# Kernel tuning notes

Hardware: AMD Instinct MI355X
Metric: run time of the kernel (lower is better)

## Reference

```python
import jax, jax.numpy as jnp
import numpy as np

IN_DIMS = 512
TOKEN_DIM = 512
NUM_HEADS = 1
D = TOKEN_DIM * NUM_HEADS
SCALE = TOKEN_DIM ** (-0.5)
EPS = 1e-12  # torch F.normalize default


def _l2norm(v, axis):
    n = jnp.sqrt(jnp.sum(v * v, axis=axis, keepdims=True))
    return v / jnp.maximum(n, EPS)


def setup_inputs() -> dict:
    key = jax.random.key(0)
    ks = jax.random.split(key, 10)
    B, C, H, W = 64, IN_DIMS, 28, 28
    s_in = IN_DIMS ** -0.5
    s_d = D ** -0.5
    return {
        "x": jax.random.normal(ks[0], (B, C, H, W), jnp.float32),
        "Wq": jax.random.normal(ks[1], (IN_DIMS, D), jnp.float32) * s_in,
        "bq": jax.random.normal(ks[2], (D,), jnp.float32) * 0.01,
        "Wk": jax.random.normal(ks[3], (IN_DIMS, D), jnp.float32) * s_in,
        "bk": jax.random.normal(ks[4], (D,), jnp.float32) * 0.01,
        "w_g": jax.random.normal(ks[5], (D, 1), jnp.float32),
        "Wp": jax.random.normal(ks[6], (D, D), jnp.float32) * s_d,
        "bp": jax.random.normal(ks[7], (D,), jnp.float32) * 0.01,
        "Wf": jax.random.normal(ks[8], (D, TOKEN_DIM), jnp.float32) * s_d,
        "bf": jax.random.normal(ks[9], (TOKEN_DIM,), jnp.float32) * 0.01,
    }


def reference(x, Wq, bq, Wk, bk, w_g, Wp, bp, Wf, bf):
    B, C, H, W = x.shape
    t = x.reshape(B, C, H * W).transpose(0, 2, 1)          # [B, N, C]
    query = _l2norm(t @ Wq + bq, axis=-1)                  # [B, N, D]
    k = _l2norm(t @ Wk + bk, axis=-1)                      # [B, N, D]
    attn = _l2norm((query @ w_g) * SCALE, axis=1)          # [B, N, 1], normalized over tokens
    ctx = jnp.sum(attn * query, axis=1, keepdims=True)     # [B, 1, D] global context
    out = (ctx * k) @ Wp + bp + query                      # [B, N, D]
    out = out @ Wf + bf                                    # [B, N, TOKEN_DIM]
    return out.transpose(0, 2, 1).reshape(B, -1, H, W)
```

## Files before the change

### kernel.cpp

```cpp
#include <hip/hip_runtime.h>

#define EPSN 1e-12f
#define SCALE_F 0.044194173824159216f

typedef __bf16 bf16x8 __attribute__((ext_vector_type(8)));
typedef float  f32x4  __attribute__((ext_vector_type(4)));

__global__ __launch_bounds__(256) void k_prep_t(const float* __restrict__ Wq,
                                                const float* __restrict__ Wk,
                                                __bf16* __restrict__ WqT,
                                                __bf16* __restrict__ WkT) {
  int idx = blockIdx.x * 256 + threadIdx.x;
  int d = idx >> 9, c = idx & 511;
  WqT[idx] = (__bf16)Wq[c * 512 + d];
  WkT[idx] = (__bf16)Wk[c * 512 + d];
}

__global__ __launch_bounds__(512) void k_prep_w(const float* __restrict__ Wp,
                                                const float* __restrict__ Wf,
                                                const float* __restrict__ bp,
                                                const float* __restrict__ bfv,
                                                __bf16* __restrict__ WcT,
                                                float* __restrict__ bpf) {
  int kk = blockIdx.x;
  int d  = threadIdx.x;
  float acc = 0.f;
  for (int c = 0; c < 512; ++c) acc = fmaf(Wp[kk * 512 + c], Wf[c * 512 + d], acc);
  WcT[(size_t)d * 1024 + kk]       = (__bf16)acc;
  WcT[(size_t)d * 1024 + 512 + kk] = (__bf16)Wf[kk * 512 + d];
  if (kk == 0) {
    float a2 = 0.f;
    for (int c = 0; c < 512; ++c) a2 = fmaf(bp[c], Wf[c * 512 + d], a2);
    bpf[d] = a2 + bfv[d];
  }
}

__global__ __launch_bounds__(512) void k_qk(const float* __restrict__ x,
                                            const __bf16* __restrict__ WqT,
                                            const __bf16* __restrict__ WkT,
                                            const float* __restrict__ bq,
                                            const float* __restrict__ bk,
                                            const float* __restrict__ wg,
                                            __bf16* __restrict__ Qn,
                                            __bf16* __restrict__ Kn,
                                            float* __restrict__ g) {
  __shared__ __bf16 As[64][40];
  __shared__ float redQ[8][64], redK[8][64], redG[8][64];
  __shared__ float invq[64], invk[64];
  const int t = threadIdx.x;
  const int lane = t & 63, w = t >> 6;
  const int li = lane & 15, lq = lane >> 4;
  const int n0 = blockIdx.x * 64;
  const int b  = blockIdx.y;
  const int sn = t & 63;
  const int sc = t >> 6;
  f32x4 accQ[4][4] = {}, accK[4][4] = {};
  for (int ks = 0; ks < 16; ++ks) {
    const int c0 = ks * 32;
    #pragma unroll
    for (int p = 0; p < 4; ++p) {
      int c = sc + p * 8;
      float v = 0.f;
      if (n0 + sn < 784) v = x[((size_t)b * 512 + c0 + c) * 784 + n0 + sn];
      As[sn][c] = (__bf16)v;
    }
    __syncthreads();
    bf16x8 af[4];
    #pragma unroll
    for (int rb = 0; rb < 4; ++rb)
      af[rb] = *(const bf16x8*)&As[rb * 16 + li][lq * 8];
    #pragma unroll
    for (int cb = 0; cb < 4; ++cb) {
      const int drow = w * 64 + cb * 16 + li;
      bf16x8 bqf = *(const bf16x8*)(WqT + (size_t)drow * 512 + c0 + lq * 8);
      bf16x8 bkf = *(const bf16x8*)(WkT + (size_t)drow * 512 + c0 + lq * 8);
      #pragma unroll
      for (int rb = 0; rb < 4; ++rb) {
        accQ[rb][cb] = __builtin_amdgcn_mfma_f32_16x16x32_bf16(af[rb], bqf, accQ[rb][cb], 0, 0, 0);
        accK[rb][cb] = __builtin_amdgcn_mfma_f32_16x16x32_bf16(af[rb], bkf, accK[rb][cb], 0, 0, 0);
      }
    }
    __syncthreads();
  }
  float bqv[4], bkv[4], wgv[4];
  #pragma unroll
  for (int cb = 0; cb < 4; ++cb) {
    int col = w * 64 + cb * 16 + li;
    bqv[cb] = bq[col]; bkv[cb] = bk[col]; wgv[cb] = wg[col];
  }
  #pragma unroll
  for (int rb = 0; rb < 4; ++rb)
    #pragma unroll
    for (int cb = 0; cb < 4; ++cb)
      #pragma unroll
      for (int j = 0; j < 4; ++j) {
        accQ[rb][cb][j] += bqv[cb];
        accK[rb][cb][j] += bkv[cb];
      }
  #pragma unroll
  for (int rb = 0; rb < 4; ++rb)
    #pragma unroll
    for (int j = 0; j < 4; ++j) {
      float sq = 0.f, sk = 0.f, sg = 0.f;
      #pragma unroll
      for (int cb = 0; cb < 4; ++cb) {
        float vq = accQ[rb][cb][j], vk = accK[rb][cb][j];
        sq = fmaf(vq, vq, sq); sk = fmaf(vk, vk, sk); sg = fmaf(vq, wgv[cb], sg);
      }
      sq += __shfl_xor(sq, 1); sq += __shfl_xor(sq, 2); sq += __shfl_xor(sq, 4); sq += __shfl_xor(sq, 8);
      sk += __shfl_xor(sk, 1); sk += __shfl_xor(sk, 2); sk += __shfl_xor(sk, 4); sk += __shfl_xor(sk, 8);
      sg += __shfl_xor(sg, 1); sg += __shfl_xor(sg, 2); sg += __shfl_xor(sg, 4); sg += __shfl_xor(sg, 8);
      if (li == 0) {
        int row = rb * 16 + lq * 4 + j;
        redQ[w][row] = sq; redK[w][row] = sk; redG[w][row] = sg;
      }
    }
  __syncthreads();
  if (t < 64) {
    float sq = 0.f, sk = 0.f, sg = 0.f;
    #pragma unroll
    for (int wv = 0; wv < 8; ++wv) { sq += redQ[wv][t]; sk += redK[wv][t]; sg += redG[wv][t]; }
    float iq = 1.f / fmaxf(sqrtf(sq), EPSN);
    float ik = 1.f / fmaxf(sqrtf(sk), EPSN);
    invq[t] = iq; invk[t] = ik;
    if (n0 + t < 784) g[(size_t)b * 784 + n0 + t] = sg * iq;
  }
  __syncthreads();
  #pragma unroll
  for (int rb = 0; rb < 4; ++rb)
    #pragma unroll
    for (int j = 0; j < 4; ++j) {
      int row = rb * 16 + lq * 4 + j;
      if (n0 + row < 784) {
        float iq = invq[row], ik = invk[row];
        size_t base = ((size_t)b * 784 + n0 + row) * 512 + w * 64 + li;
        #pragma unroll
        for (int cb = 0; cb < 4; ++cb) {
          Qn[base + cb * 16] = (__bf16)(accQ[rb][cb][j] * iq);
          Kn[base + cb * 16] = (__bf16)(accK[rb][cb][j] * ik);
        }
      }
    }
}

__global__ __launch_bounds__(512) void k_ctx(const __bf16* __restrict__ Qn,
                                             const float* __restrict__ g,
                                             float* __restrict__ ctx) {
  const int b = blockIdx.x, t = threadIdx.x;
  __shared__ float wred[8];
  const float* gb = g + (size_t)b * 784;
  float s = 0.f;
  for (int n = t; n < 784; n += 512) { float v = gb[n]; s = fmaf(v, v, s); }
  s += __shfl_xor(s, 1);  s += __shfl_xor(s, 2);  s += __shfl_xor(s, 4);
  s += __shfl_xor(s, 8);  s += __shfl_xor(s, 16); s += __shfl_xor(s, 32);
  if ((t & 63) == 0) wred[t >> 6] = s;
  __syncthreads();
  float tot = 0.f;
  #pragma unroll
  for (int i = 0; i < 8; ++i) tot += wred[i];
  float alpha = SCALE_F / fmaxf(sqrtf(tot) * SCALE_F, EPSN);
  const __bf16* qb = Qn + (size_t)b * 784 * 512;
  float a0 = 0.f, a1 = 0.f, a2 = 0.f, a3 = 0.f;
  for (int n = 0; n < 784; n += 4) {
    a0 = fmaf(gb[n],     (float)qb[(size_t)n * 512 + t],       a0);
    a1 = fmaf(gb[n + 1], (float)qb[(size_t)(n + 1) * 512 + t], a1);
    a2 = fmaf(gb[n + 2], (float)qb[(size_t)(n + 2) * 512 + t], a2);
    a3 = fmaf(gb[n + 3], (float)qb[(size_t)(n + 3) * 512 + t], a3);
  }
  ctx[(size_t)b * 512 + t] = alpha * ((a0 + a1) + (a2 + a3));
}

__global__ __launch_bounds__(512) void k_out(const __bf16* __restrict__ Qn,
                                             const __bf16* __restrict__ Kn,
                                             const float* __restrict__ ctx,
                                             const __bf16* __restrict__ WcT,
                                             const float* __restrict__ bpf,
                                             float* __restrict__ out) {
  __shared__ __align__(16) char smem[64 * 72 * 2 + 256 * 72 * 2];
  __bf16 (*As)[72] = (__bf16(*)[72])smem;
  __bf16 (*Bs)[72] = (__bf16(*)[72])(smem + 64 * 72 * 2);
  float  (*Cs)[65] = (float(*)[65])smem;
  const int t = threadIdx.x;
  const int lane = t & 63, w = t >> 6;
  const int li = lane & 15, lq = lane >> 4;
  const int wr = w >> 2, wc = w & 3;
  const int n0 = blockIdx.x * 64;
  const int d0 = blockIdx.y * 256;
  const int b  = blockIdx.z;
  const int arow = t >> 3, asg = t & 7;
  f32x4 acc[2][4] = {};
  for (int ks = 0; ks < 16; ++ks) {
    const int k0 = ks * 64;
    {
      int kk = k0 + asg * 8;
      int n = n0 + arow;
      bf16x8 v = {};
      if (kk < 512) {
        if (n < 784) v = *(const bf16x8*)(Kn + ((size_t)b * 784 + n) * 512 + kk);
        const float* cp = ctx + b * 512 + kk;
        bf16x8 r;
        #pragma unroll
        for (int j = 0; j < 8; ++j) r[j] = (__bf16)((float)v[j] * cp[j]);
        *(bf16x8*)&As[arow][asg * 8] = r;
      } else {
        if (n < 784) v = *(const bf16x8*)(Qn + ((size_t)b * 784 + n) * 512 + kk - 512);
        *(bf16x8*)&As[arow][asg * 8] = v;
      }
    }
    #pragma unroll
    for (int p = 0; p < 4; ++p) {
      int d = (t >> 3) + p * 64;
      *(bf16x8*)&Bs[d][asg * 8] = *(const bf16x8*)(WcT + (size_t)(d0 + d) * 1024 + k0 + asg * 8);
    }
    __syncthreads();
    bf16x8 af[2][2], bfr[4][2];
    #pragma unroll
    for (int rb = 0; rb < 2; ++rb)
      #pragma unroll
      for (int kf = 0; kf < 2; ++kf)
        af[rb][kf] = *(const bf16x8*)&As[wr * 32 + rb * 16 + li][kf * 32 + lq * 8];
    #pragma unroll
    for (int cb = 0; cb < 4; ++cb)
      #pragma unroll
      for (int kf = 0; kf < 2; ++kf)
        bfr[cb][kf] = *(const bf16x8*)&Bs[wc * 64 + cb * 16 + li][kf * 32 + lq * 8];
    #pragma unroll
    for (int kf = 0; kf < 2; ++kf)
      #pragma unroll
      for (int rb = 0; rb < 2; ++rb)
        #pragma unroll
        for (int cb = 0; cb < 4; ++cb)
          acc[rb][cb] = __builtin_amdgcn_mfma_f32_16x16x32_bf16(af[rb][kf], bfr[cb][kf], acc[rb][cb], 0, 0, 0);
    __syncthreads();
  }
  for (int ch = 0; ch < 4; ++ch) {
    if (wc == ch) {
      #pragma unroll
      for (int cb = 0; cb < 4; ++cb) {
        int colL = cb * 16 + li;
        float bias = bpf[d0 + ch * 64 + colL];
        #pragma unroll
        for (int rb = 0; rb < 2; ++rb)
          #pragma unroll
          for (int j = 0; j < 4; ++j)
            Cs[colL][wr * 32 + rb * 16 + lq * 4 + j] = acc[rb][cb][j] + bias;
      }
    }
    __syncthreads();
    {
      int n = t & 63, dl = t >> 6;
      if (n0 + n < 784) {
        #pragma unroll
        for (int p = 0; p < 8; ++p)
          out[((size_t)b * 512 + d0 + ch * 64 + dl + p * 8) * 784 + n0 + n] = Cs[dl + p * 8][n];
      }
    }
    __syncthreads();
  }
}

extern "C" void kernel_launch(void* const* d_in, const int* in_sizes, int n_in,
                              void* d_out, int out_size, void* d_ws, size_t ws_size,
                              hipStream_t stream) {
  const float* x   = (const float*)d_in[0];
  const float* Wq  = (const float*)d_in[1];
  const float* bq  = (const float*)d_in[2];
  const float* Wk  = (const float*)d_in[3];
  const float* bk  = (const float*)d_in[4];
  const float* wg  = (const float*)d_in[5];
  const float* Wp  = (const float*)d_in[6];
  const float* bp  = (const float*)d_in[7];
  const float* Wf  = (const float*)d_in[8];
  const float* bfv = (const float*)d_in[9];
  float* out = (float*)d_out;
  char* ws = (char*)d_ws;

  const size_t SZQN = (size_t)64 * 784 * 512 * 2;
  __bf16* Qn   = (__bf16*)(ws);
  __bf16* Kn   = (__bf16*)(ws + SZQN);
  __bf16* WqT  = (__bf16*)(ws + 2 * SZQN);
  __bf16* WkT  = (__bf16*)(ws + 2 * SZQN + 524288);
  __bf16* WcT  = (__bf16*)(ws + 2 * SZQN + 2 * 524288);
  float*  gbuf = (float*) (ws + 2 * SZQN + 2 * 524288 + 1048576);
  float*  ctx  = (float*) (ws + 2 * SZQN + 2 * 524288 + 1048576 + 200704);
  float*  bpf  = (float*) (ws + 2 * SZQN + 2 * 524288 + 1048576 + 200704 + 131072);

  k_prep_t<<<dim3(1024), dim3(256), 0, stream>>>(Wq, Wk, WqT, WkT);
  k_prep_w<<<dim3(512),  dim3(512), 0, stream>>>(Wp, Wf, bp, bfv, WcT, bpf);
  k_qk   <<<dim3(13, 64),    dim3(512), 0, stream>>>(x, WqT, WkT, bq, bk, wg, Qn, Kn, gbuf);
  k_ctx  <<<dim3(64),        dim3(512), 0, stream>>>(Qn, gbuf, ctx);
  k_out  <<<dim3(13, 2, 64), dim3(512), 0, stream>>>(Qn, Kn, ctx, WcT, bpf, out);
}
```

Baseline: 432.1 us.

## Double-buffer GEMM staging, split context reduction, and coalesce weight prep

k_qk and k_out now prefetch the next K-slices of activations and weights into registers and ping-pong two LDS buffers, so global loads overlap the MFMA work and each step needs one barrier. The context reduction is split into a 7-way partial pass over token chunks plus a small combine kernel. Before, it ran as only 64 blocks that each walked 784 rows, so parallelism was poor. k_prep_t becomes a coalesced shared-memory tiled transpose, and k_prep_w gets multiple accumulators. The partial buffers reuse the WqT/WkT workspace, which adds register pressure (hence the occupancy hint) and an extra launch.

```diff
diff --git a/kernel.cpp b/kernel.cpp
--- a/kernel.cpp
+++ b/kernel.cpp
@@ -4,16 +4,29 @@
 #define SCALE_F 0.044194173824159216f
 
 typedef __bf16 bf16x8 __attribute__((ext_vector_type(8)));
+typedef __bf16 bf16x4 __attribute__((ext_vector_type(4)));
 typedef float  f32x4  __attribute__((ext_vector_type(4)));
 
 __global__ __launch_bounds__(256) void k_prep_t(const float* __restrict__ Wq,
                                                 const float* __restrict__ Wk,
                                                 __bf16* __restrict__ WqT,
                                                 __bf16* __restrict__ WkT) {
-  int idx = blockIdx.x * 256 + threadIdx.x;
-  int d = idx >> 9, c = idx & 511;
-  WqT[idx] = (__bf16)Wq[c * 512 + d];
-  WkT[idx] = (__bf16)Wk[c * 512 + d];
+  __shared__ float Tq[32][33], Tk[32][33];
+  const int c0 = blockIdx.x * 32, d0 = blockIdx.y * 32;
+  const int dx = threadIdx.x, cy = threadIdx.y;
+  #pragma unroll
+  for (int p = 0; p < 4; ++p) {
+    int c = cy + p * 8;
+    Tq[c][dx] = Wq[(size_t)(c0 + c) * 512 + d0 + dx];
+    Tk[c][dx] = Wk[(size_t)(c0 + c) * 512 + d0 + dx];
+  }
+  __syncthreads();
+  #pragma unroll
+  for (int p = 0; p < 4; ++p) {
+    int d = cy + p * 8;
+    WqT[(size_t)(d0 + d) * 512 + c0 + dx] = (__bf16)Tq[dx][d];
+    WkT[(size_t)(d0 + d) * 512 + c0 + dx] = (__bf16)Tk[dx][d];
+  }
 }
 
 __global__ __launch_bounds__(512) void k_prep_w(const float* __restrict__ Wp,
@@ -24,27 +37,35 @@
                                                 float* __restrict__ bpf) {
   int kk = blockIdx.x;
   int d  = threadIdx.x;
-  float acc = 0.f;
-  for (int c = 0; c < 512; ++c) acc = fmaf(Wp[kk * 512 + c], Wf[c * 512 + d], acc);
-  WcT[(size_t)d * 1024 + kk]       = (__bf16)acc;
-  WcT[(size_t)d * 1024 + 512 + kk] = (__bf16)Wf[kk * 512 + d];
+  float a0 = 0.f, a1 = 0.f, a2 = 0.f, a3 = 0.f;
+  for (int c = 0; c < 512; c += 4) {
+    a0 = fmaf(Wp[kk * 512 + c],     Wf[(size_t)c * 512 + d],         a0);
+    a1 = fmaf(Wp[kk * 512 + c + 1], Wf[(size_t)(c + 1) * 512 + d],   a1);
+    a2 = fmaf(Wp[kk * 512 + c + 2], Wf[(size_t)(c + 2) * 512 + d],   a2);
+    a3 = fmaf(Wp[kk * 512 + c + 3], Wf[(size_t)(c + 3) * 512 + d],   a3);
+  }
+  WcT[(size_t)d * 1024 + kk]       = (__bf16)((a0 + a1) + (a2 + a3));
+  WcT[(size_t)d * 1024 + 512 + kk] = (__bf16)Wf[(size_t)kk * 512 + d];
   if (kk == 0) {
-    float a2 = 0.f;
-    for (int c = 0; c < 512; ++c) a2 = fmaf(bp[c], Wf[c * 512 + d], a2);
-    bpf[d] = a2 + bfv[d];
-  }
-}
-
-__global__ __launch_bounds__(512) void k_qk(const float* __restrict__ x,
-                                            const __bf16* __restrict__ WqT,
-                                            const __bf16* __restrict__ WkT,
-                                            const float* __restrict__ bq,
-                                            const float* __restrict__ bk,
-                                            const float* __restrict__ wg,
-                                            __bf16* __restrict__ Qn,
-                                            __bf16* __restrict__ Kn,
-                                            float* __restrict__ g) {
-  __shared__ __bf16 As[64][40];
+    float b0 = 0.f, b1 = 0.f;
+    for (int c = 0; c < 512; c += 2) {
+      b0 = fmaf(bp[c],     Wf[(size_t)c * 512 + d],       b0);
+      b1 = fmaf(bp[c + 1], Wf[(size_t)(c + 1) * 512 + d], b1);
+    }
+    bpf[d] = b0 + b1 + bfv[d];
+  }
+}
+
+__global__ __launch_bounds__(512, 2) void k_qk(const float* __restrict__ x,
+                                               const __bf16* __restrict__ WqT,
+                                               const __bf16* __restrict__ WkT,
+                                               const float* __restrict__ bq,
+                                               const float* __restrict__ bk,
+                                               const float* __restrict__ wg,
+                                               __bf16* __restrict__ Qn,
+                                               __bf16* __restrict__ Kn,
+                                               float* __restrict__ g) {
+  __shared__ __bf16 As[2][64][36];
   __shared__ float redQ[8][64], redK[8][64], redG[8][64];
   __shared__ float invq[64], invk[64];
   const int t = threadIdx.x;
@@ -52,36 +73,59 @@
   const int li = lane & 15, lq = lane >> 4;
   const int n0 = blockIdx.x * 64;
   const int b  = blockIdx.y;
-  const int sn = t & 63;
-  const int sc = t >> 6;
+  const int sn = t & 63, sc4 = (t >> 6) * 4;
+  const bool nv = (n0 + sn < 784);
+  const float* xp = x + ((size_t)b * 512 + sc4) * 784 + n0 + sn;
+  const __bf16* wqp = WqT + (size_t)(w * 64 + li) * 512 + lq * 8;
+  const __bf16* wkp = WkT + (size_t)(w * 64 + li) * 512 + lq * 8;
+
   f32x4 accQ[4][4] = {}, accK[4][4] = {};
+  bf16x8 bq2[2][4], bk2[2][4];
+  float xr[2][4];
+
+  auto issueX = [&](int set, int ks) {
+    #pragma unroll
+    for (int j = 0; j < 4; ++j)
+      xr[set][j] = nv ? xp[(size_t)(ks * 32 + j) * 784] : 0.f;
+  };
+  auto issueB = [&](int set, int ks) {
+    #pragma unroll
+    for (int cb = 0; cb < 4; ++cb) {
+      bq2[set][cb] = *(const bf16x8*)(wqp + (size_t)cb * 8192 + ks * 32);
+      bk2[set][cb] = *(const bf16x8*)(wkp + (size_t)cb * 8192 + ks * 32);
+    }
+  };
+  auto writeA = [&](int buf, int set) {
+    bf16x4 v;
+    #pragma unroll
+    for (int j = 0; j < 4; ++j) v[j] = (__bf16)xr[set][j];
+    *(bf16x4*)&As[buf][sn][sc4] = v;
+  };
+
+  issueX(0, 0); issueX(1, 1); issueB(0, 0);
+  writeA(0, 0);
+  __syncthreads();
+
+  #pragma unroll
   for (int ks = 0; ks < 16; ++ks) {
-    const int c0 = ks * 32;
-    #pragma unroll
-    for (int p = 0; p < 4; ++p) {
-      int c = sc + p * 8;
-      float v = 0.f;
-      if (n0 + sn < 784) v = x[((size_t)b * 512 + c0 + c) * 784 + n0 + sn];
-      As[sn][c] = (__bf16)v;
-    }
+    const int cur = ks & 1, nxt = cur ^ 1;
+    if (ks + 2 < 16) issueX(cur, ks + 2);
+    if (ks + 1 < 16) issueB(nxt, ks + 1);
+    bf16x8 af[4];
+    #pragma unroll
+    for (int rb = 0; rb < 4; ++rb)
+      af[rb] = *(const bf16x8*)&As[cur][rb * 16 + li][lq * 8];
+    #pragma unroll
+    for (int cb = 0; cb < 4; ++cb)
+      #pragma unroll
+      for (int rb = 0; rb < 4; ++rb) {
+        accQ[rb][cb] = __builtin_amdgcn_mfma_f32_16x16x32_bf16(af[rb], bq2[cur][cb], accQ[rb][cb], 0, 0, 0);
+        accK[rb][cb] = __builtin_amdgcn_mfma_f32_16x16x32_bf16(af[rb], bk2[cur][cb], accK[rb][cb], 0, 0, 0);
+      }
+    if (ks + 1 < 16) writeA(nxt, nxt);
     __syncthreads();
-    bf16x8 af[4];
-    #pragma unroll
-    for (int rb = 0; rb < 4; ++rb)
-      af[rb] = *(const bf16x8*)&As[rb * 16 + li][lq * 8];
-    #pragma unroll
-    for (int cb = 0; cb < 4; ++cb) {
-      const int drow = w * 64 + cb * 16 + li;
-      bf16x8 bqf = *(const bf16x8*)(WqT + (size_t)drow * 512 + c0 + lq * 8);
-      bf16x8 bkf = *(const bf16x8*)(WkT + (size_t)drow * 512 + c0 + lq * 8);
-      #pragma unroll
-      for (int rb = 0; rb < 4; ++rb) {
-        accQ[rb][cb] = __builtin_amdgcn_mfma_f32_16x16x32_bf16(af[rb], bqf, accQ[rb][cb], 0, 0, 0);
-        accK[rb][cb] = __builtin_amdgcn_mfma_f32_16x16x32_bf16(af[rb], bkf, accK[rb][cb], 0, 0, 0);
-      }
-    }
-    __syncthreads();
-  }
+  }
+
   float bqv[4], bkv[4], wgv[4];
   #pragma unroll
   for (int cb = 0; cb < 4; ++cb) {
@@ -143,31 +187,51 @@
     }
 }
 
-__global__ __launch_bounds__(512) void k_ctx(const __bf16* __restrict__ Qn,
-                                             const float* __restrict__ g,
-                                             float* __restrict__ ctx) {
-  const int b = blockIdx.x, t = threadIdx.x;
+__global__ __launch_bounds__(512) void k_ctx1(const __bf16* __restrict__ Qn,
+                                              const float* __restrict__ g,
+                                              float* __restrict__ pctx,
+                                              float* __restrict__ pgsq) {
+  const int cx = blockIdx.x;
+  const int b  = blockIdx.y;
+  const int t  = threadIdx.x;
+  const int nbase = cx * 112;
   __shared__ float wred[8];
-  const float* gb = g + (size_t)b * 784;
+  const float* gb = g + (size_t)b * 784 + nbase;
   float s = 0.f;
-  for (int n = t; n < 784; n += 512) { float v = gb[n]; s = fmaf(v, v, s); }
+  if (t < 112) { float v = gb[t]; s = v * v; }
   s += __shfl_xor(s, 1);  s += __shfl_xor(s, 2);  s += __shfl_xor(s, 4);
   s += __shfl_xor(s, 8);  s += __shfl_xor(s, 16); s += __shfl_xor(s, 32);
   if ((t & 63) == 0) wred[t >> 6] = s;
   __syncthreads();
+  if (t == 0) {
+    float tot = 0.f;
+    #pragma unroll
+    for (int i = 0; i < 8; ++i) tot += wred[i];
+    pgsq[b * 7 + cx] = tot;
+  }
+  const __bf16* qb = Qn + ((size_t)b * 784 + nbase) * 512 + t;
+  float a0 = 0.f, a1 = 0.f, a2 = 0.f, a3 = 0.f;
+  for (int n = 0; n < 112; n += 4) {
+    a0 = fmaf(gb[n],     (float)qb[(size_t)n * 512],       a0);
+    a1 = fmaf(gb[n + 1], (float)qb[(size_t)(n + 1) * 512], a1);
+    a2 = fmaf(gb[n + 2], (float)qb[(size_t)(n + 2) * 512], a2);
+    a3 = fmaf(gb[n + 3], (float)qb[(size_t)(n + 3) * 512], a3);
+  }
+  pctx[((size_t)b * 7 + cx) * 512 + t] = (a0 + a1) + (a2 + a3);
+}
+
+__global__ __launch_bounds__(512) void k_ctx2(const float* __restrict__ pctx,
+                                              const float* __restrict__ pgsq,
+                                              float* __restrict__ ctx) {
+  const int b = blockIdx.x, t = threadIdx.x;
   float tot = 0.f;
   #pragma unroll
-  for (int i = 0; i < 8; ++i) tot += wred[i];
+  for (int i = 0; i < 7; ++i) tot += pgsq[b * 7 + i];
   float alpha = SCALE_F / fmaxf(sqrtf(tot) * SCALE_F, EPSN);
-  const __bf16* qb = Qn + (size_t)b * 784 * 512;
-  float a0 = 0.f, a1 = 0.f, a2 = 0.f, a3 = 0.f;
-  for (int n = 0; n < 784; n += 4) {
-    a0 = fmaf(gb[n],     (float)qb[(size_t)n * 512 + t],       a0);
-    a1 = fmaf(gb[n + 1], (float)qb[(size_t)(n + 1) * 512 + t], a1);
-    a2 = fmaf(gb[n + 2], (float)qb[(size_t)(n + 2) * 512 + t], a2);
-    a3 = fmaf(gb[n + 3], (float)qb[(size_t)(n + 3) * 512 + t], a3);
-  }
-  ctx[(size_t)b * 512 + t] = alpha * ((a0 + a1) + (a2 + a3));
+  float s = 0.f;
+  #pragma unroll
+  for (int i = 0; i < 7; ++i) s += pctx[((size_t)b * 7 + i) * 512 + t];
+  ctx[(size_t)b * 512 + t] = alpha * s;
 }
 
 __global__ __launch_bounds__(512) void k_out(const __bf16* __restrict__ Qn,
@@ -176,10 +240,10 @@
                                              const __bf16* __restrict__ WcT,
                                              const float* __restrict__ bpf,
                                              float* __restrict__ out) {
-  __shared__ __align__(16) char smem[64 * 72 * 2 + 256 * 72 * 2];
-  __bf16 (*As)[72] = (__bf16(*)[72])smem;
-  __bf16 (*Bs)[72] = (__bf16(*)[72])(smem + 64 * 72 * 2);
-  float  (*Cs)[65] = (float(*)[65])smem;
+  __shared__ __align__(16) char smem[(2 * 64 * 36 + 2 * 256 * 36) * 2];
+  __bf16 (*As)[64][36]  = (__bf16(*)[64][36])smem;
+  __bf16 (*Bs)[256][36] = (__bf16(*)[256][36])(smem + 2 * 64 * 36 * 2);
+  float  (*Cs)[65]      = (float(*)[65])smem;
   const int t = threadIdx.x;
   const int lane = t & 63, w = t >> 6;
   const int li = lane & 15, lq = lane >> 4;
@@ -187,52 +251,72 @@
   const int n0 = blockIdx.x * 64;
   const int d0 = blockIdx.y * 256;
   const int b  = blockIdx.z;
-  const int arow = t >> 3, asg = t & 7;
+  const int an = t & 63, ak4 = (t >> 6) * 4;
+  const bool anv = (n0 + an < 784);
+  const __bf16* qrow = Qn + ((size_t)b * 784 + n0 + an) * 512;
+  const __bf16* krow = Kn + ((size_t)b * 784 + n0 + an) * 512;
+  const float* cxp = ctx + (size_t)b * 512;
+  const int br = t >> 2, bc8 = (t & 3) * 8;
+  const __bf16* wp0 = WcT + (size_t)(d0 + br) * 1024 + bc8;
+  const __bf16* wp1 = WcT + (size_t)(d0 + br + 128) * 1024 + bc8;
+
   f32x4 acc[2][4] = {};
-  for (int ks = 0; ks < 16; ++ks) {
-    const int k0 = ks * 64;
-    {
-      int kk = k0 + asg * 8;
-      int n = n0 + arow;
-      bf16x8 v = {};
-      if (kk < 512) {
-        if (n < 784) v = *(const bf16x8*)(Kn + ((size_t)b * 784 + n) * 512 + kk);
-        const float* cp = ctx + b * 512 + kk;
-        bf16x8 r;
-        #pragma unroll
-        for (int j = 0; j < 8; ++j) r[j] = (__bf16)((float)v[j] * cp[j]);
-        *(bf16x8*)&As[arow][asg * 8] = r;
-      } else {
-        if (n < 784) v = *(const bf16x8*)(Qn + ((size_t)b * 784 + n) * 512 + kk - 512);
-        *(bf16x8*)&As[arow][asg * 8] = v;
-      }
-    }
-    #pragma unroll
-    for (int p = 0; p < 4; ++p) {
-      int d = (t >> 3) + p * 64;
-      *(bf16x8*)&Bs[d][asg * 8] = *(const bf16x8*)(WcT + (size_t)(d0 + d) * 1024 + k0 + asg * 8);
-    }
+  bf16x4 aqk[2];
+  f32x4 cx4[2];
+  bf16x8 bw[2][2];
+
+  auto issueA = [&](int set, int ks) {
+    int kk = ks * 32 + ak4;
+    bf16x4 v = {};
+    if (ks < 16) {
+      if (anv) v = *(const bf16x4*)(krow + kk);
+      cx4[set] = *(const f32x4*)(cxp + kk);
+    } else {
+      if (anv) v = *(const bf16x4*)(qrow + kk - 512);
+    }
+    aqk[set] = v;
+  };
+  auto issueB = [&](int set, int ks) {
+    bw[set][0] = *(const bf16x8*)(wp0 + ks * 32);
+    bw[set][1] = *(const bf16x8*)(wp1 + ks * 32);
+  };
+  auto writeAB = [&](int buf, int set, int ks) {
+    bf16x4 v;
+    if (ks < 16) {
+      #pragma unroll
+      for (int j = 0; j < 4; ++j) v[j] = (__bf16)((float)aqk[set][j] * cx4[set][j]);
+    } else {
+      v = aqk[set];
+    }
+    *(bf16x4*)&As[buf][an][ak4] = v;
+    *(bf16x8*)&Bs[buf][br][bc8]       = bw[set][0];
+    *(bf16x8*)&Bs[buf][br + 128][bc8] = bw[set][1];
+  };
+
+  issueA(0, 0); issueB(0, 0); issueA(1, 1); issueB(1, 1);
+  writeAB(0, 0, 0);
+  __syncthreads();
+
+  #pragma unroll
+  for (int ks = 0; ks < 32; ++ks) {
+    const int cur = ks & 1, nxt = cur ^ 1;
+    if (ks + 2 < 32) { issueA(cur, ks + 2); issueB(cur, ks + 2); }
+    bf16x8 af[2], bf[4];
+    #pragma unroll
+    for (int rb = 0; rb < 2; ++rb)
+      af[rb] = *(const bf16x8*)&As[cur][wr * 32 + rb * 16 + li][lq * 8];
+    #pragma unroll
+    for (int cb = 0; cb < 4; ++cb)
+      bf[cb] = *(const bf16x8*)&Bs[cur][wc * 64 + cb * 16 + li][lq * 8];
+    #pragma unroll
+    for (int cb = 0; cb < 4; ++cb)
+      #pragma unroll
+      for (int rb = 0; rb < 2; ++rb)
+        acc[rb][cb] = __builtin_amdgcn_mfma_f32_16x16x32_bf16(af[rb], bf[cb], acc[rb][cb], 0, 0, 0);
+    if (ks + 1 < 32) writeAB(nxt, nxt, ks + 1);
     __syncthreads();
-    bf16x8 af[2][2], bfr[4][2];
-    #pragma unroll
-    for (int rb = 0; rb < 2; ++rb)
-      #pragma unroll
-      for (int kf = 0; kf < 2; ++kf)
-        af[rb][kf] = *(const bf16x8*)&As[wr * 32 + rb * 16 + li][kf * 32 + lq * 8];
-    #pragma unroll
-    for (int cb = 0; cb < 4; ++cb)
-      #pragma unroll
-      for (int kf = 0; kf < 2; ++kf)
-        bfr[cb][kf] = *(const bf16x8*)&Bs[wc * 64 + cb * 16 + li][kf * 32 + lq * 8];
-    #pragma unroll
-    for (int kf = 0; kf < 2; ++kf)
-      #pragma unroll
-      for (int rb = 0; rb < 2; ++rb)
-        #pragma unroll
-        for (int cb = 0; cb < 4; ++cb)
-          acc[rb][cb] = __builtin_amdgcn_mfma_f32_16x16x32_bf16(af[rb][kf], bfr[cb][kf], acc[rb][cb], 0, 0, 0);
-    __syncthreads();
-  }
+  }
+
   for (int ch = 0; ch < 4; ++ch) {
     if (wc == ch) {
       #pragma unroll
@@ -284,10 +368,13 @@
   float*  gbuf = (float*) (ws + 2 * SZQN + 2 * 524288 + 1048576);
   float*  ctx  = (float*) (ws + 2 * SZQN + 2 * 524288 + 1048576 + 200704);
   float*  bpf  = (float*) (ws + 2 * SZQN + 2 * 524288 + 1048576 + 200704 + 131072);
-
-  k_prep_t<<<dim3(1024), dim3(256), 0, stream>>>(Wq, Wk, WqT, WkT);
-  k_prep_w<<<dim3(512),  dim3(512), 0, stream>>>(Wp, Wf, bp, bfv, WcT, bpf);
-  k_qk   <<<dim3(13, 64),    dim3(512), 0, stream>>>(x, WqT, WkT, bq, bk, wg, Qn, Kn, gbuf);
-  k_ctx  <<<dim3(64),        dim3(512), 0, stream>>>(Qn, gbuf, ctx);
-  k_out  <<<dim3(13, 2, 64), dim3(512), 0, stream>>>(Qn, Kn, ctx, WcT, bpf, out);
-}
+  float*  pctx = (float*)(ws + 2 * SZQN);
+  float*  pgsq = (float*)(ws + 2 * SZQN + 917504);
+
+  k_prep_t<<<dim3(16, 16),    dim3(32, 8), 0, stream>>>(Wq, Wk, WqT, WkT);
+  k_prep_w<<<dim3(512),       dim3(512),   0, stream>>>(Wp, Wf, bp, bfv, WcT, bpf);
+  k_qk    <<<dim3(13, 64),    dim3(512),   0, stream>>>(x, WqT, WkT, bq, bk, wg, Qn, Kn, gbuf);
+  k_ctx1  <<<dim3(7, 64),     dim3(512),   0, stream>>>(Qn, gbuf, pctx, pgsq);
+  k_ctx2  <<<dim3(64),        dim3(512),   0, stream>>>(pctx, pgsq, ctx);
+  k_out   <<<dim3(13, 2, 64), dim3(512),   0, stream>>>(Qn, Kn, ctx, WcT, bpf, out);
+}
```

New measurement: 690.0 us. 1.6x slower.
